# Kernel optimization log

Measured on AMD Instinct MI355X. Metric: run time of the kernel, lower is better.

## Reference

```python
import jax, jax.numpy as jnp
import numpy as np

N = 10000
E = 160000
H = 4
NEG_SLOPE = 0.2


def _edge_softmax(e, dst):
    # e: [E, H] logits; softmax over edges sharing the same dst node
    m = jax.ops.segment_max(e, dst, num_segments=N)          # [N, H]
    m = jnp.where(jnp.isfinite(m), m, 0.0)
    ex = jnp.exp(e - m[dst])                                  # [E, H]
    den = jax.ops.segment_sum(ex, dst, num_segments=N)       # [N, H]
    return ex / (den[dst] + 1e-9)


def _gat_layer(x, src, dst, W, al, ar, resW, edge=None, We=None, ae=None):
    # x: [N, Fin]; W: [Fin, H, D]; al/ar/ae: [H, D]; resW: [Fin, D]
    feat = jnp.einsum('ni,ihd->nhd', x, W)                    # [N, H, D]
    el = jnp.einsum('nhd,hd->nh', feat, al)                   # [N, H]
    er = jnp.einsum('nhd,hd->nh', feat, ar)                   # [N, H]
    e = el[src] + er[dst]                                     # [E, H]
    if edge is not None:
        ef = jnp.einsum('ei,ihd->ehd', edge, We)              # [E, H, D]
        e = e + jnp.einsum('ehd,hd->eh', ef, ae)
    e = jax.nn.leaky_relu(e, NEG_SLOPE)
    alpha = _edge_softmax(e, dst)                             # [E, H]
    msg = feat[src] * alpha[:, :, None]                       # [E, H, D]
    out = jax.ops.segment_sum(msg, dst, num_segments=N)      # [N, H, D]
    return out.mean(axis=1) + x @ resW                        # [N, D]


def setup_inputs() -> dict:
    key = jax.random.key(0)
    ks = jax.random.split(key, 24)
    node_in, edge_in, hid, out = 128, 64, 128, 256
    s = 0.1
    d = {
        'node_feats': jax.random.normal(ks[0], (N, node_in), jnp.float32),
        'edge_feats': jax.random.normal(ks[1], (E, edge_in), jnp.float32),
        'src': jax.random.randint(ks[2], (E,), 0, N, jnp.int32),
        'dst': jax.random.randint(ks[3], (E,), 0, N, jnp.int32),
        # conv1 (with edge feats): node_in -> hid
        'W1':  s * jax.random.normal(ks[4],  (node_in, H, hid), jnp.float32),
        'We1': s * jax.random.normal(ks[5],  (edge_in, H, hid), jnp.float32),
        'al1': s * jax.random.normal(ks[6],  (H, hid), jnp.float32),
        'ar1': s * jax.random.normal(ks[7],  (H, hid), jnp.float32),
        'ae1': s * jax.random.normal(ks[8],  (H, hid), jnp.float32),
        'res1': s * jax.random.normal(ks[9], (node_in, hid), jnp.float32),
        # conv2: hid -> hid
        'W2':  s * jax.random.normal(ks[10], (hid, H, hid), jnp.float32),
        'al2': s * jax.random.normal(ks[11], (H, hid), jnp.float32),
        'ar2': s * jax.random.normal(ks[12], (H, hid), jnp.float32),
        'res2': s * jax.random.normal(ks[13], (hid, hid), jnp.float32),
        # conv3: hid -> hid
        'W3':  s * jax.random.normal(ks[14], (hid, H, hid), jnp.float32),
        'al3': s * jax.random.normal(ks[15], (H, hid), jnp.float32),
        'ar3': s * jax.random.normal(ks[16], (H, hid), jnp.float32),
        'res3': s * jax.random.normal(ks[17], (hid, hid), jnp.float32),
        # conv4: hid -> out
        'W4':  s * jax.random.normal(ks[18], (hid, H, out), jnp.float32),
        'al4': s * jax.random.normal(ks[19], (H, out), jnp.float32),
        'ar4': s * jax.random.normal(ks[20], (H, out), jnp.float32),
        'res4': s * jax.random.normal(ks[21], (hid, out), jnp.float32),
    }
    return d


def reference(node_feats, edge_feats, src, dst,
              W1, We1, al1, ar1, ae1, res1,
              W2, al2, ar2, res2,
              W3, al3, ar3, res3,
              W4, al4, ar4, res4):
    h = jax.nn.relu(_gat_layer(node_feats, src, dst, W1, al1, ar1, res1,
                               edge=edge_feats, We=We1, ae=ae1))
    h = jax.nn.relu(_gat_layer(h, src, dst, W2, al2, ar2, res2))
    h = jax.nn.relu(_gat_layer(h, src, dst, W3, al3, ar3, res3))
    h = jax.nn.relu(_gat_layer(h, src, dst, W4, al4, ar4, res4))
    return h
```

## Files before the change

kernel.cpp:

```cpp
#include <hip/hip_runtime.h>

#define NN 10000
#define EE 160000

typedef __attribute__((ext_vector_type(8))) short bf16x8;
typedef __attribute__((ext_vector_type(4))) float f32x4;

__device__ __forceinline__ float b2f(unsigned short s) {
    union { unsigned u; float f; } v; v.u = ((unsigned)s) << 16; return v.f;
}
__device__ __forceinline__ short f2b(float f) {
    union { float f; unsigned u; } v; v.f = f;
    unsigned r = v.u + 0x7FFF + ((v.u >> 16) & 1);
    return (short)(r >> 16);
}

__global__ __launch_bounds__(256) void hist_kernel(const int* __restrict__ dst,
                                                   int* __restrict__ counts, int E) {
    int e = blockIdx.x * 256 + threadIdx.x;
    if (e < E) atomicAdd(&counts[dst[e]], 1);
}

__global__ __launch_bounds__(256) void scan_kernel(const int* __restrict__ counts,
                                                   int* __restrict__ off,
                                                   int* __restrict__ cur, int n) {
    __shared__ int buf[NN];
    __shared__ int part[256];
    int tid = threadIdx.x;
    for (int j = tid; j < n; j += 256) buf[j] = counts[j];
    __syncthreads();
    int chunk = (n + 255) / 256;
    int lo = tid * chunk; if (lo > n) lo = n;
    int hi = lo + chunk;  if (hi > n) hi = n;
    int s = 0;
    for (int i = lo; i < hi; ++i) s += buf[i];
    part[tid] = s;
    __syncthreads();
    for (int o = 1; o < 256; o <<= 1) {
        int v = (tid >= o) ? part[tid - o] : 0;
        __syncthreads();
        part[tid] += v;
        __syncthreads();
    }
    int run = (tid == 0) ? 0 : part[tid - 1];
    for (int i = lo; i < hi; ++i) { int c = buf[i]; buf[i] = run; run += c; }
    __syncthreads();
    for (int j = tid; j < n; j += 256) { int v = buf[j]; off[j] = v; cur[j] = v; }
    if (tid == 255) off[n] = part[255];
}

__global__ __launch_bounds__(256) void fill_extra(const int* __restrict__ src,
                                                  const int* __restrict__ dst,
                                                  int* __restrict__ cur,
                                                  const float* __restrict__ ef,
                                                  const float* __restrict__ vbuf,
                                                  int* __restrict__ ssrc,
                                                  float* __restrict__ extra, int E) {
    __shared__ float vs[256];
    vs[threadIdx.x] = vbuf[threadIdx.x];
    __syncthreads();
    int e = blockIdx.x * 256 + threadIdx.x;
    if (e >= E) return;
    int p = atomicAdd(&cur[dst[e]], 1);
    ssrc[p] = src[e];
    float a0 = 0.f, a1 = 0.f, a2 = 0.f, a3 = 0.f;
    const float4* e4 = (const float4*)(ef + (size_t)e * 64);
    #pragma unroll
    for (int c = 0; c < 16; ++c) {
        float4 x = e4[c];
        int b = c * 16;
        a0 += x.x * vs[b + 0] + x.y * vs[b + 4] + x.z * vs[b + 8] + x.w * vs[b + 12];
        a1 += x.x * vs[b + 1] + x.y * vs[b + 5] + x.z * vs[b + 9] + x.w * vs[b + 13];
        a2 += x.x * vs[b + 2] + x.y * vs[b + 6] + x.z * vs[b + 10] + x.w * vs[b + 14];
        a3 += x.x * vs[b + 3] + x.y * vs[b + 7] + x.z * vs[b + 11] + x.w * vs[b + 15];
    }
    float4 o; o.x = a0; o.y = a1; o.z = a2; o.w = a3;
    *(float4*)(extra + (size_t)p * 4) = o;
}

struct PrepParams {
    const float* tsrc[8];
    short* tdst[8];
    int tN[8];
    int tshift[8];
    int tcum4[9];
    const float* W[4]; const float* al[4]; const float* ar[4];
    short* Wc[4]; int Dl[4]; int base[4];
    const float* We1; const float* ae1; float* vbuf;
    const float* node_feats; short* xb;
    int* counts;
    int bWA, bV, bC, bZ;
};
__global__ __launch_bounds__(256) void prep_kernel(PrepParams P) {
    int blk = blockIdx.x, tid = threadIdx.x;
    if (blk < P.bWA) {
        int t = blk * 256 + tid;
        if (t >= P.tcum4[8]) return;
        int i = 0;
        #pragma unroll
        for (int j = 1; j < 8; ++j) i += (t >= P.tcum4[j]);
        int local = t - P.tcum4[i];
        int N = P.tN[i], sh = P.tshift[i];
        int k = local >> (sh - 2);
        int nq = local & ((N >> 2) - 1);
        float4 v = *(const float4*)(P.tsrc[i] + (size_t)k * N + nq * 4);
        short* d = P.tdst[i] + (size_t)nq * 4 * 128 + k;
        d[0] = f2b(v.x); d[128] = f2b(v.y); d[256] = f2b(v.z); d[384] = f2b(v.w);
    } else if (blk < P.bV) {
        int bl = blk - P.bWA;
        int l = bl >> 7, within = bl & 127;
        int wv = tid >> 6, ln = tid & 63;
        int wid = within * 4 + wv;
        int k = wid >> 2, h = wid & 3;
        int D = P.Dl[l];
        const float* w = P.W[l] + ((size_t)k * 4 + h) * D;
        const float* a = P.al[l] + (size_t)h * D;
        const float* r = P.ar[l] + (size_t)h * D;
        float sa, sr;
        if (D == 128) {
            float2 w2 = ((const float2*)w)[ln];
            float2 a2 = ((const float2*)a)[ln];
            float2 r2 = ((const float2*)r)[ln];
            sa = w2.x * a2.x + w2.y * a2.y;
            sr = w2.x * r2.x + w2.y * r2.y;
        } else {
            float4 w4 = ((const float4*)w)[ln];
            float4 a4 = ((const float4*)a)[ln];
            float4 r4 = ((const float4*)r)[ln];
            sa = w4.x * a4.x + w4.y * a4.y + w4.z * a4.z + w4.w * a4.w;
            sr = w4.x * r4.x + w4.y * r4.y + w4.z * r4.z + w4.w * r4.w;
        }
        #pragma unroll
        for (int o = 32; o; o >>= 1) { sa += __shfl_xor(sa, o); sr += __shfl_xor(sr, o); }
        if (ln == 0) {
            P.Wc[l][(size_t)(P.base[l] + h) * 128 + k]     = f2b(sa);
            P.Wc[l][(size_t)(P.base[l] + 4 + h) * 128 + k] = f2b(sr);
        }
    } else if (blk < P.bC) {
        int bl = blk - P.bV;
        int wv = tid >> 6, ln = tid & 63;
        int i = bl * 4 + wv;
        #pragma unroll
        for (int h = 0; h < 4; ++h) {
            const float* w = P.We1 + ((size_t)i * 4 + h) * 128;
            const float* a = P.ae1 + (size_t)h * 128;
            float2 w2 = ((const float2*)w)[ln];
            float2 a2 = ((const float2*)a)[ln];
            float s = w2.x * a2.x + w2.y * a2.y;
            #pragma unroll
            for (int o = 32; o; o >>= 1) s += __shfl_xor(s, o);
            if (ln == 0) P.vbuf[i * 4 + h] = s;
        }
    } else if (blk < P.bZ) {
        int t = (blk - P.bC) * 256 + tid;
        if (t < NN * 32) {
            float4 v = ((const float4*)P.node_feats)[t];
            uint2 pk;
            pk.x = (unsigned short)f2b(v.x) | ((unsigned)(unsigned short)f2b(v.y) << 16);
            pk.y = (unsigned short)f2b(v.z) | ((unsigned)(unsigned short)f2b(v.w) << 16);
            ((uint2*)P.xb)[t] = pk;
        }
    } else {
        int t = (blk - P.bZ) * 256 + tid;
        if (t < NN / 4) ((int4*)P.counts)[t] = make_int4(0, 0, 0, 0);
    }
}

template <int D>
__global__ __launch_bounds__(256) void gemm_fused(const short* __restrict__ A,
                                                  const short* __restrict__ Bt,
                                                  short* __restrict__ featb,
                                                  float* __restrict__ y,
                                                  float* __restrict__ elr,
                                                  int M) {
    constexpr int HD = 4 * D;
    int wave = threadIdx.x >> 6, lane = threadIdx.x & 63;
    int m0 = blockIdx.y * 64;
    int n0 = blockIdx.x * 64 + wave * 16;
    int r = lane & 15, quad = lane >> 4;
    f32x4 acc[4] = {};
    const short* bp = Bt + (size_t)(n0 + r) * 128 + quad * 8;
    #pragma unroll
    for (int k0 = 0; k0 < 128; k0 += 32) {
        bf16x8 bfrag = *(const bf16x8*)(bp + k0);
        #pragma unroll
        for (int mt = 0; mt < 4; ++mt) {
            int gm = m0 + mt * 16 + r;
            bf16x8 afrag = {};
            if (gm < M) afrag = *(const bf16x8*)(A + (size_t)gm * 128 + k0 + quad * 8);
            acc[mt] = __builtin_amdgcn_mfma_f32_16x16x32_bf16(afrag, bfrag, acc[mt], 0, 0, 0);
        }
    }
    int col = n0 + r;
    #pragma unroll
    for (int mt = 0; mt < 4; ++mt) {
        #pragma unroll
        for (int rr = 0; rr < 4; ++rr) {
            int gm = m0 + mt * 16 + quad * 4 + rr;
            if (gm >= M) continue;
            float v = acc[mt][rr];
            if (col < HD)              featb[(size_t)gm * HD + col] = f2b(v);
            else if (col < HD + D)     y[(size_t)gm * D + (col - HD)] = v;
            else if (col < HD + D + 8) elr[(size_t)gm * 8 + (col - HD - D)] = v;
        }
    }
}

__device__ __forceinline__ void accum8(float* a, uint4 v, float w) {
    a[0] += w * b2f((unsigned short)(v.x & 0xFFFF));
    a[1] += w * b2f((unsigned short)(v.x >> 16));
    a[2] += w * b2f((unsigned short)(v.y & 0xFFFF));
    a[3] += w * b2f((unsigned short)(v.y >> 16));
    a[4] += w * b2f((unsigned short)(v.z & 0xFFFF));
    a[5] += w * b2f((unsigned short)(v.z >> 16));
    a[6] += w * b2f((unsigned short)(v.w & 0xFFFF));
    a[7] += w * b2f((unsigned short)(v.w >> 16));
}

template <int CH>
__device__ __forceinline__ void gather_chunk(int cnt, int sidx,
                                             float e0, float e1, float e2, float e3,
                                             const short* __restrict__ featb, int ln,
                                             float acc[CH][8]) {
    constexpr int HD = CH * 512;
    const short* base = featb + ln * 8;
    int j = 0;
    for (; j + 2 <= cnt; j += 2) {
        int sA = __shfl(sidx, j), sB = __shfl(sidx, j + 1);
        float wA0 = __shfl(e0, j), wA1 = __shfl(e1, j), wA2 = __shfl(e2, j), wA3 = __shfl(e3, j);
        float wB0 = __shfl(e0, j + 1), wB1 = __shfl(e1, j + 1), wB2 = __shfl(e2, j + 1), wB3 = __shfl(e3, j + 1);
        const short* fA = base + (size_t)sA * HD;
        const short* fB = base + (size_t)sB * HD;
        uint4 vA[CH], vB[CH];
        #pragma unroll
        for (int c = 0; c < CH; ++c) { vA[c] = *(const uint4*)(fA + c * 512); vB[c] = *(const uint4*)(fB + c * 512); }
        #pragma unroll
        for (int c = 0; c < CH; ++c) {
            float wA, wB;
            if (CH == 1) {
                wA = ln < 16 ? wA0 : ln < 32 ? wA1 : ln < 48 ? wA2 : wA3;
                wB = ln < 16 ? wB0 : ln < 32 ? wB1 : ln < 48 ? wB2 : wB3;
            } else {
                wA = (c == 0) ? (ln < 32 ? wA0 : wA1) : (ln < 32 ? wA2 : wA3);
                wB = (c == 0) ? (ln < 32 ? wB0 : wB1) : (ln < 32 ? wB2 : wB3);
            }
            accum8(acc[c], vA[c], wA);
            accum8(acc[c], vB[c], wB);
        }
    }
    if (j < cnt) {
        int sA = __shfl(sidx, j);
        float wA0 = __shfl(e0, j), wA1 = __shfl(e1, j), wA2 = __shfl(e2, j), wA3 = __shfl(e3, j);
        const short* fA = base + (size_t)sA * HD;
        #pragma unroll
        for (int c = 0; c < CH; ++c) {
            uint4 vA = *(const uint4*)(fA + c * 512);
            float wA;
            if (CH == 1) wA = ln < 16 ? wA0 : ln < 32 ? wA1 : ln < 48 ? wA2 : wA3;
            else         wA = (c == 0) ? (ln < 32 ? wA0 : wA1) : (ln < 32 ? wA2 : wA3);
            accum8(acc[c], vA, wA);
        }
    }
}

template <int D, bool HAS_EXTRA, bool WRITE_BF>
__global__ __launch_bounds__(256) void gat_wave(const short* __restrict__ featb,
                                                const float* __restrict__ elr,
                                                const float* __restrict__ extra,
                                                const int* __restrict__ ssrc,
                                                const int* __restrict__ off,
                                                const float* __restrict__ yres,
                                                float* __restrict__ yout,
                                                short* __restrict__ ybf) {
    constexpr int HD = 4 * D;
    constexpr int CH = HD / 512;
    int wv = threadIdx.x >> 6, ln = threadIdx.x & 63;
    int n = blockIdx.x * 4 + wv;
    int r0 = off[n], deg = off[n + 1] - r0;

    float4 erv = *(const float4*)(elr + (size_t)n * 8 + 4);

    float acc[CH][8];
    #pragma unroll
    for (int c = 0; c < CH; ++c)
        #pragma unroll
        for (int i = 0; i < 8; ++i) acc[c][i] = 0.f;

    float sc0, sc1, sc2, sc3;

    auto logits = [&](int idx, float& a0, float& a1, float& a2, float& a3) {
        int s = ssrc[idx];
        float4 elv = *(const float4*)(elr + (size_t)s * 8);
        a0 = elv.x + erv.x; a1 = elv.y + erv.y; a2 = elv.z + erv.z; a3 = elv.w + erv.w;
        if (HAS_EXTRA) {
            float4 exv = *(const float4*)(extra + (size_t)idx * 4);
            a0 += exv.x; a1 += exv.y; a2 += exv.z; a3 += exv.w;
        }
        a0 = a0 > 0.f ? a0 : 0.2f * a0;
        a1 = a1 > 0.f ? a1 : 0.2f * a1;
        a2 = a2 > 0.f ? a2 : 0.2f * a2;
        a3 = a3 > 0.f ? a3 : 0.2f * a3;
        return s;
    };

    if (deg <= 64) {
        int sidx = 0;
        float a0 = -1e30f, a1 = -1e30f, a2 = -1e30f, a3 = -1e30f;
        if (ln < deg) sidx = logits(r0 + ln, a0, a1, a2, a3);
        float m0 = a0, m1 = a1, m2 = a2, m3 = a3;
        #pragma unroll
        for (int o = 32; o; o >>= 1) {
            m0 = fmaxf(m0, __shfl_xor(m0, o)); m1 = fmaxf(m1, __shfl_xor(m1, o));
            m2 = fmaxf(m2, __shfl_xor(m2, o)); m3 = fmaxf(m3, __shfl_xor(m3, o));
        }
        float e0 = 0.f, e1 = 0.f, e2 = 0.f, e3 = 0.f;
        if (ln < deg) {
            e0 = __expf(a0 - m0); e1 = __expf(a1 - m1);
            e2 = __expf(a2 - m2); e3 = __expf(a3 - m3);
        }
        float s0 = e0, s1 = e1, s2 = e2, s3 = e3;
        #pragma unroll
        for (int o = 32; o; o >>= 1) {
            s0 += __shfl_xor(s0, o); s1 += __shfl_xor(s1, o);
            s2 += __shfl_xor(s2, o); s3 += __shfl_xor(s3, o);
        }
        sc0 = 0.25f / (s0 + 1e-9f); sc1 = 0.25f / (s1 + 1e-9f);
        sc2 = 0.25f / (s2 + 1e-9f); sc3 = 0.25f / (s3 + 1e-9f);
        gather_chunk<CH>(deg, sidx, e0, e1, e2, e3, featb, ln, acc);
    } else {
        float m0 = -1e30f, m1 = -1e30f, m2 = -1e30f, m3 = -1e30f;
        for (int base = 0; base < deg; base += 64) {
            float a0 = -1e30f, a1 = -1e30f, a2 = -1e30f, a3 = -1e30f;
            if (base + ln < deg) logits(r0 + base + ln, a0, a1, a2, a3);
            m0 = fmaxf(m0, a0); m1 = fmaxf(m1, a1); m2 = fmaxf(m2, a2); m3 = fmaxf(m3, a3);
        }
        #pragma unroll
        for (int o = 32; o; o >>= 1) {
            m0 = fmaxf(m0, __shfl_xor(m0, o)); m1 = fmaxf(m1, __shfl_xor(m1, o));
            m2 = fmaxf(m2, __shfl_xor(m2, o)); m3 = fmaxf(m3, __shfl_xor(m3, o));
        }
        float s0 = 0.f, s1 = 0.f, s2 = 0.f, s3 = 0.f;
        for (int base = 0; base < deg; base += 64) {
            float a0, a1, a2, a3;
            if (base + ln < deg) {
                logits(r0 + base + ln, a0, a1, a2, a3);
                s0 += __expf(a0 - m0); s1 += __expf(a1 - m1);
                s2 += __expf(a2 - m2); s3 += __expf(a3 - m3);
            }
        }
        #pragma unroll
        for (int o = 32; o; o >>= 1) {
            s0 += __shfl_xor(s0, o); s1 += __shfl_xor(s1, o);
            s2 += __shfl_xor(s2, o); s3 += __shfl_xor(s3, o);
        }
        sc0 = 0.25f / (s0 + 1e-9f); sc1 = 0.25f / (s1 + 1e-9f);
        sc2 = 0.25f / (s2 + 1e-9f); sc3 = 0.25f / (s3 + 1e-9f);
        for (int base = 0; base < deg; base += 64) {
            int sidx = 0;
            float e0 = 0.f, e1 = 0.f, e2 = 0.f, e3 = 0.f;
            if (base + ln < deg) {
                float a0, a1, a2, a3;
                sidx = logits(r0 + base + ln, a0, a1, a2, a3);
                e0 = __expf(a0 - m0); e1 = __expf(a1 - m1);
                e2 = __expf(a2 - m2); e3 = __expf(a3 - m3);
            }
            int cnt = deg - base; if (cnt > 64) cnt = 64;
            gather_chunk<CH>(cnt, sidx, e0, e1, e2, e3, featb, ln, acc);
        }
    }

    if (CH == 1) {
        float scl = ln < 16 ? sc0 : ln < 32 ? sc1 : ln < 48 ? sc2 : sc3;
        float t[8];
        #pragma unroll
        for (int i = 0; i < 8; ++i) {
            float v = acc[0][i] * scl;
            v += __shfl_xor(v, 16);
            v += __shfl_xor(v, 32);
            t[i] = v;
        }
        if (ln < 16) {
            int d0 = ln * 8;
            const float* yr = yres + (size_t)n * D + d0;
            float4 ya = *(const float4*)yr;
            float4 yb = *(const float4*)(yr + 4);
            float o[8];
            o[0] = fmaxf(ya.x + t[0], 0.f); o[1] = fmaxf(ya.y + t[1], 0.f);
            o[2] = fmaxf(ya.z + t[2], 0.f); o[3] = fmaxf(ya.w + t[3], 0.f);
            o[4] = fmaxf(yb.x + t[4], 0.f); o[5] = fmaxf(yb.y + t[5], 0.f);
            o[6] = fmaxf(yb.z + t[6], 0.f); o[7] = fmaxf(yb.w + t[7], 0.f);
            if (WRITE_BF) {
                uint4 pk;
                pk.x = (unsigned short)f2b(o[0]) | ((unsigned)(unsigned short)f2b(o[1]) << 16);
                pk.y = (unsigned short)f2b(o[2]) | ((unsigned)(unsigned short)f2b(o[3]) << 16);
                pk.z = (unsigned short)f2b(o[4]) | ((unsigned)(unsigned short)f2b(o[5]) << 16);
                pk.w = (unsigned short)f2b(o[6]) | ((unsigned)(unsigned short)f2b(o[7]) << 16);
                *(uint4*)(ybf + (size_t)n * D + d0) = pk;
            } else {
                float4 oa, ob;
                oa.x = o[0]; oa.y = o[1]; oa.z = o[2]; oa.w = o[3];
                ob.x = o[4]; ob.y = o[5]; ob.z = o[6]; ob.w = o[7];
                *(float4*)(yout + (size_t)n * D + d0) = oa;
                *(float4*)(yout + (size_t)n * D + d0 + 4) = ob;
            }
        }
    } else {
        float scA = ln < 32 ? sc0 : sc1;
        float scB = ln < 32 ? sc2 : sc3;
        float t[8];
        #pragma unroll
        for (int i = 0; i < 8; ++i) {
            float v = acc[0][i] * scA + acc[1][i] * scB;
            v += __shfl_xor(v, 32);
            t[i] = v;
        }
        if (ln < 32) {
            int d0 = ln * 8;
            const float* yr = yres + (size_t)n * D + d0;
            float4 ya = *(const float4*)yr;
            float4 yb = *(const float4*)(yr + 4);
            float o[8];
            o[0] = fmaxf(ya.x + t[0], 0.f); o[1] = fmaxf(ya.y + t[1], 0.f);
            o[2] = fmaxf(ya.z + t[2], 0.f); o[3] = fmaxf(ya.w + t[3], 0.f);
            o[4] = fmaxf(yb.x + t[4], 0.f); o[5] = fmaxf(yb.y + t[5], 0.f);
            o[6] = fmaxf(yb.z + t[6], 0.f); o[7] = fmaxf(yb.w + t[7], 0.f);
            if (WRITE_BF) {
                uint4 pk;
                pk.x = (unsigned short)f2b(o[0]) | ((unsigned)(unsigned short)f2b(o[1]) << 16);
                pk.y = (unsigned short)f2b(o[2]) | ((unsigned)(unsigned short)f2b(o[3]) << 16);
                pk.z = (unsigned short)f2b(o[4]) | ((unsigned)(unsigned short)f2b(o[5]) << 16);
                pk.w = (unsigned short)f2b(o[6]) | ((unsigned)(unsigned short)f2b(o[7]) << 16);
                *(uint4*)(ybf + (size_t)n * D + d0) = pk;
            } else {
                float4 oa, ob;
                oa.x = o[0]; oa.y = o[1]; oa.z = o[2]; oa.w = o[3];
                ob.x = o[4]; ob.y = o[5]; ob.z = o[6]; ob.w = o[7];
                *(float4*)(yout + (size_t)n * D + d0) = oa;
                *(float4*)(yout + (size_t)n * D + d0 + 4) = ob;
            }
        }
    }
}

extern "C" void kernel_launch(void* const* d_in, const int* in_sizes, int n_in,
                              void* d_out, int out_size, void* d_ws, size_t ws_size,
                              hipStream_t stream) {
    const float* node_feats = (const float*)d_in[0];
    const float* edge_feats = (const float*)d_in[1];
    const int*   src        = (const int*)d_in[2];
    const int*   dst        = (const int*)d_in[3];
    const float* W1   = (const float*)d_in[4];
    const float* We1  = (const float*)d_in[5];
    const float* al1  = (const float*)d_in[6];
    const float* ar1  = (const float*)d_in[7];
    const float* ae1  = (const float*)d_in[8];
    const float* res1 = (const float*)d_in[9];
    const float* W2   = (const float*)d_in[10];
    const float* al2  = (const float*)d_in[11];
    const float* ar2  = (const float*)d_in[12];
    const float* res2 = (const float*)d_in[13];
    const float* W3   = (const float*)d_in[14];
    const float* al3  = (const float*)d_in[15];
    const float* ar3  = (const float*)d_in[16];
    const float* res3 = (const float*)d_in[17];
    const float* W4   = (const float*)d_in[18];
    const float* al4  = (const float*)d_in[19];
    const float* ar4  = (const float*)d_in[20];
    const float* res4 = (const float*)d_in[21];

    char* ws = (char*)d_ws;
    auto alloc = [&](size_t bytes) -> char* {
        char* p = ws;
        ws += (bytes + 255) & ~(size_t)255;
        return p;
    };
    int*   counts  = (int*)alloc((size_t)NN * 4);
    int*   offsets = (int*)alloc((size_t)(NN + 1) * 4);
    int*   cursor  = (int*)alloc((size_t)(NN + 1) * 4);
    int*   ssrc    = (int*)alloc((size_t)EE * 4);
    short* featb   = (short*)alloc((size_t)NN * 1024 * 2);
    float* xA      = (float*)alloc((size_t)NN * 128 * 4);
    short* xb      = (short*)alloc((size_t)NN * 128 * 2);
    float* elr     = (float*)alloc((size_t)NN * 8 * 4);
    float* extra   = (float*)alloc((size_t)EE * 4 * 4);
    float* vbuf    = (float*)alloc(1024);
    short* Wc1     = (short*)alloc((size_t)704 * 128 * 2);
    short* Wc2     = (short*)alloc((size_t)704 * 128 * 2);
    short* Wc3     = (short*)alloc((size_t)704 * 128 * 2);
    short* Wc4     = (short*)alloc((size_t)1344 * 128 * 2);

    PrepParams P;
    P.tsrc[0] = W1;   P.tdst[0] = Wc1;              P.tN[0] = 512;  P.tshift[0] = 9;
    P.tsrc[1] = W2;   P.tdst[1] = Wc2;              P.tN[1] = 512;  P.tshift[1] = 9;
    P.tsrc[2] = W3;   P.tdst[2] = Wc3;              P.tN[2] = 512;  P.tshift[2] = 9;
    P.tsrc[3] = W4;   P.tdst[3] = Wc4;              P.tN[3] = 1024; P.tshift[3] = 10;
    P.tsrc[4] = res1; P.tdst[4] = Wc1 + 512 * 128;  P.tN[4] = 128;  P.tshift[4] = 7;
    P.tsrc[5] = res2; P.tdst[5] = Wc2 + 512 * 128;  P.tN[5] = 128;  P.tshift[5] = 7;
    P.tsrc[6] = res3; P.tdst[6] = Wc3 + 512 * 128;  P.tN[6] = 128;  P.tshift[6] = 7;
    P.tsrc[7] = res4; P.tdst[7] = Wc4 + 1024 * 128; P.tN[7] = 256;  P.tshift[7] = 8;
    P.tcum4[0] = 0;
    for (int i = 0; i < 8; ++i) P.tcum4[i + 1] = P.tcum4[i] + P.tN[i] * 128 / 4;
    P.W[0] = W1; P.W[1] = W2; P.W[2] = W3; P.W[3] = W4;
    P.al[0] = al1; P.al[1] = al2; P.al[2] = al3; P.al[3] = al4;
    P.ar[0] = ar1; P.ar[1] = ar2; P.ar[2] = ar3; P.ar[3] = ar4;
    P.Wc[0] = Wc1; P.Wc[1] = Wc2; P.Wc[2] = Wc3; P.Wc[3] = Wc4;
    P.Dl[0] = 128; P.Dl[1] = 128; P.Dl[2] = 128; P.Dl[3] = 256;
    P.base[0] = 640; P.base[1] = 640; P.base[2] = 640; P.base[3] = 1280;
    P.We1 = We1; P.ae1 = ae1; P.vbuf = vbuf;
    P.node_feats = node_feats; P.xb = xb;
    P.counts = counts;
    P.bWA = (P.tcum4[8] + 255) / 256;
    P.bV  = P.bWA + 512;
    P.bC  = P.bV + 16;
    P.bZ  = P.bC + (NN * 32 + 255) / 256;
    int nblk = P.bZ + (NN / 4 + 255) / 256;
    prep_kernel<<<nblk, 256, 0, stream>>>(P);

    hist_kernel<<<(EE + 255) / 256, 256, 0, stream>>>(dst, counts, EE);
    scan_kernel<<<1, 256, 0, stream>>>(counts, offsets, cursor, NN);
    fill_extra<<<(EE + 255) / 256, 256, 0, stream>>>(src, dst, cursor, edge_feats,
                                                     vbuf, ssrc, extra, EE);

    float* out = (float*)d_out;
    dim3 g128(11, (NN + 63) / 64);
    dim3 g256(21, (NN + 63) / 64);
    int gw = NN / 4;

    gemm_fused<128><<<g128, 256, 0, stream>>>(xb, Wc1, featb, xA, elr, NN);
    gat_wave<128, true, true><<<gw, 256, 0, stream>>>(featb, elr, extra, ssrc, offsets, xA, nullptr, xb);
    gemm_fused<128><<<g128, 256, 0, stream>>>(xb, Wc2, featb, xA, elr, NN);
    gat_wave<128, false, true><<<gw, 256, 0, stream>>>(featb, elr, nullptr, ssrc, offsets, xA, nullptr, xb);
    gemm_fused<128><<<g128, 256, 0, stream>>>(xb, Wc3, featb, xA, elr, NN);
    gat_wave<128, false, true><<<gw, 256, 0, stream>>>(featb, elr, nullptr, ssrc, offsets, xA, nullptr, xb);
    gemm_fused<256><<<g256, 256, 0, stream>>>(xb, Wc4, featb, out, elr, NN);
    gat_wave<256, false, false><<<gw, 256, 0, stream>>>(featb, elr, nullptr, ssrc, offsets, out, out, nullptr);
}
```

Measured before the change: 382.9 us.

## Split each node's GAT aggregation across two waves with LDS reduction

```diff
diff --git a/kernel.cpp b/kernel.cpp
--- a/kernel.cpp
+++ b/kernel.cpp
@@ -217,75 +217,89 @@
     a[7] += w * b2f((unsigned short)(v.w >> 16));
 }
 
-template <int CH>
-__device__ __forceinline__ void gather_chunk(int cnt, int sidx,
-                                             float e0, float e1, float e2, float e3,
-                                             const short* __restrict__ featb, int ln,
-                                             float acc[CH][8]) {
-    constexpr int HD = CH * 512;
-    const short* base = featb + ln * 8;
+__device__ __forceinline__ float sel4(int ln, float s0, float s1, float s2, float s3) {
+    return ln < 16 ? s0 : ln < 32 ? s1 : ln < 48 ? s2 : s3;
+}
+
+__device__ __forceinline__ void gather_q(int cnt, int start, int step, int sidx,
+                                         float e0, float e1, float e2, float e3,
+                                         const short* __restrict__ base, int ln,
+                                         float acc[8]) {
+    int j = start;
+    for (; j + 3 * step < cnt; j += 4 * step) {
+        int jB = j + step, jC = j + 2 * step, jD = j + 3 * step;
+        int s0 = __shfl(sidx, j), s1 = __shfl(sidx, jB);
+        int s2 = __shfl(sidx, jC), s3 = __shfl(sidx, jD);
+        uint4 v0 = *(const uint4*)(base + (size_t)s0 * 512);
+        uint4 v1 = *(const uint4*)(base + (size_t)s1 * 512);
+        uint4 v2 = *(const uint4*)(base + (size_t)s2 * 512);
+        uint4 v3 = *(const uint4*)(base + (size_t)s3 * 512);
+        float a00 = __shfl(e0, j),  a01 = __shfl(e1, j),  a02 = __shfl(e2, j),  a03 = __shfl(e3, j);
+        float a10 = __shfl(e0, jB), a11 = __shfl(e1, jB), a12 = __shfl(e2, jB), a13 = __shfl(e3, jB);
+        float a20 = __shfl(e0, jC), a21 = __shfl(e1, jC), a22 = __shfl(e2, jC), a23 = __shfl(e3, jC);
+        float a30 = __shfl(e0, jD), a31 = __shfl(e1, jD), a32 = __shfl(e2, jD), a33 = __shfl(e3, jD);
+        float w0 = sel4(ln, a00, a01, a02, a03);
+        float w1 = sel4(ln, a10, a11, a12, a13);
+        float w2 = sel4(ln, a20, a21, a22, a23);
+        float w3 = sel4(ln, a30, a31, a32, a33);
+        accum8(acc, v0, w0); accum8(acc, v1, w1);
+        accum8(acc, v2, w2); accum8(acc, v3, w3);
+    }
+    for (; j < cnt; j += step) {
+        int s0 = __shfl(sidx, j);
+        uint4 v0 = *(const uint4*)(base + (size_t)s0 * 512);
+        float a0 = __shfl(e0, j), a1 = __shfl(e1, j), a2 = __shfl(e2, j), a3 = __shfl(e3, j);
+        float w0 = sel4(ln, a0, a1, a2, a3);
+        accum8(acc, v0, w0);
+    }
+}
+
+__device__ __forceinline__ void gather_p(int cnt, int sidx, float eA, float eB,
+                                         const short* __restrict__ base, int ln,
+                                         float acc[8]) {
     int j = 0;
-    for (; j + 2 <= cnt; j += 2) {
-        int sA = __shfl(sidx, j), sB = __shfl(sidx, j + 1);
-        float wA0 = __shfl(e0, j), wA1 = __shfl(e1, j), wA2 = __shfl(e2, j), wA3 = __shfl(e3, j);
-        float wB0 = __shfl(e0, j + 1), wB1 = __shfl(e1, j + 1), wB2 = __shfl(e2, j + 1), wB3 = __shfl(e3, j + 1);
-        const short* fA = base + (size_t)sA * HD;
-        const short* fB = base + (size_t)sB * HD;
-        uint4 vA[CH], vB[CH];
-        #pragma unroll
-        for (int c = 0; c < CH; ++c) { vA[c] = *(const uint4*)(fA + c * 512); vB[c] = *(const uint4*)(fB + c * 512); }
-        #pragma unroll
-        for (int c = 0; c < CH; ++c) {
-            float wA, wB;
-            if (CH == 1) {
-                wA = ln < 16 ? wA0 : ln < 32 ? wA1 : ln < 48 ? wA2 : wA3;
-                wB = ln < 16 ? wB0 : ln < 32 ? wB1 : ln < 48 ? wB2 : wB3;
-            } else {
-                wA = (c == 0) ? (ln < 32 ? wA0 : wA1) : (ln < 32 ? wA2 : wA3);
-                wB = (c == 0) ? (ln < 32 ? wB0 : wB1) : (ln < 32 ? wB2 : wB3);
-            }
-            accum8(acc[c], vA[c], wA);
-            accum8(acc[c], vB[c], wB);
-        }
-    }
-    if (j < cnt) {
-        int sA = __shfl(sidx, j);
-        float wA0 = __shfl(e0, j), wA1 = __shfl(e1, j), wA2 = __shfl(e2, j), wA3 = __shfl(e3, j);
-        const short* fA = base + (size_t)sA * HD;
-        #pragma unroll
-        for (int c = 0; c < CH; ++c) {
-            uint4 vA = *(const uint4*)(fA + c * 512);
-            float wA;
-            if (CH == 1) wA = ln < 16 ? wA0 : ln < 32 ? wA1 : ln < 48 ? wA2 : wA3;
-            else         wA = (c == 0) ? (ln < 32 ? wA0 : wA1) : (ln < 32 ? wA2 : wA3);
-            accum8(acc[c], vA, wA);
-        }
-    }
-}
-
-template <int D, bool HAS_EXTRA, bool WRITE_BF>
-__global__ __launch_bounds__(256) void gat_wave(const short* __restrict__ featb,
-                                                const float* __restrict__ elr,
-                                                const float* __restrict__ extra,
-                                                const int* __restrict__ ssrc,
-                                                const int* __restrict__ off,
-                                                const float* __restrict__ yres,
-                                                float* __restrict__ yout,
-                                                short* __restrict__ ybf) {
-    constexpr int HD = 4 * D;
-    constexpr int CH = HD / 512;
+    for (; j + 4 <= cnt; j += 4) {
+        int s0 = __shfl(sidx, j), s1 = __shfl(sidx, j + 1);
+        int s2 = __shfl(sidx, j + 2), s3 = __shfl(sidx, j + 3);
+        uint4 v0 = *(const uint4*)(base + (size_t)s0 * 1024);
+        uint4 v1 = *(const uint4*)(base + (size_t)s1 * 1024);
+        uint4 v2 = *(const uint4*)(base + (size_t)s2 * 1024);
+        uint4 v3 = *(const uint4*)(base + (size_t)s3 * 1024);
+        float a0A = __shfl(eA, j),     a0B = __shfl(eB, j);
+        float a1A = __shfl(eA, j + 1), a1B = __shfl(eB, j + 1);
+        float a2A = __shfl(eA, j + 2), a2B = __shfl(eB, j + 2);
+        float a3A = __shfl(eA, j + 3), a3B = __shfl(eB, j + 3);
+        float w0 = ln < 32 ? a0A : a0B;
+        float w1 = ln < 32 ? a1A : a1B;
+        float w2 = ln < 32 ? a2A : a2B;
+        float w3 = ln < 32 ? a3A : a3B;
+        accum8(acc, v0, w0); accum8(acc, v1, w1);
+        accum8(acc, v2, w2); accum8(acc, v3, w3);
+    }
+    for (; j < cnt; ++j) {
+        int s0 = __shfl(sidx, j);
+        uint4 v0 = *(const uint4*)(base + (size_t)s0 * 1024);
+        float aA = __shfl(eA, j), aB = __shfl(eB, j);
+        float w0 = ln < 32 ? aA : aB;
+        accum8(acc, v0, w0);
+    }
+}
+
+template <bool HAS_EXTRA>
+__global__ __launch_bounds__(256) void gat128(const short* __restrict__ featb,
+                                              const float* __restrict__ elr,
+                                              const float* __restrict__ extra,
+                                              const int* __restrict__ ssrc,
+                                              const int* __restrict__ off,
+                                              const float* __restrict__ yres,
+                                              short* __restrict__ ybf) {
+    __shared__ float red[2][128];
     int wv = threadIdx.x >> 6, ln = threadIdx.x & 63;
-    int n = blockIdx.x * 4 + wv;
+    int slot = wv >> 1, half = wv & 1;
+    int n = blockIdx.x * 2 + slot;
     int r0 = off[n], deg = off[n + 1] - r0;
-
     float4 erv = *(const float4*)(elr + (size_t)n * 8 + 4);
-
-    float acc[CH][8];
-    #pragma unroll
-    for (int c = 0; c < CH; ++c)
-        #pragma unroll
-        for (int i = 0; i < 8; ++i) acc[c][i] = 0.f;
-
+    float acc[8] = {0.f, 0.f, 0.f, 0.f, 0.f, 0.f, 0.f, 0.f};
     float sc0, sc1, sc2, sc3;
 
     auto logits = [&](int idx, float& a0, float& a1, float& a2, float& a3) {
@@ -326,7 +340,7 @@
         }
         sc0 = 0.25f / (s0 + 1e-9f); sc1 = 0.25f / (s1 + 1e-9f);
         sc2 = 0.25f / (s2 + 1e-9f); sc3 = 0.25f / (s3 + 1e-9f);
-        gather_chunk<CH>(deg, sidx, e0, e1, e2, e3, featb, ln, acc);
+        gather_q(deg, half, 2, sidx, e0, e1, e2, e3, featb + ln * 8, ln, acc);
     } else {
         float m0 = -1e30f, m1 = -1e30f, m2 = -1e30f, m3 = -1e30f;
         for (int base = 0; base < deg; base += 64) {
@@ -365,80 +379,173 @@
                 e2 = __expf(a2 - m2); e3 = __expf(a3 - m3);
             }
             int cnt = deg - base; if (cnt > 64) cnt = 64;
-            gather_chunk<CH>(cnt, sidx, e0, e1, e2, e3, featb, ln, acc);
-        }
-    }
-
-    if (CH == 1) {
-        float scl = ln < 16 ? sc0 : ln < 32 ? sc1 : ln < 48 ? sc2 : sc3;
-        float t[8];
-        #pragma unroll
-        for (int i = 0; i < 8; ++i) {
-            float v = acc[0][i] * scl;
-            v += __shfl_xor(v, 16);
-            v += __shfl_xor(v, 32);
-            t[i] = v;
-        }
-        if (ln < 16) {
-            int d0 = ln * 8;
-            const float* yr = yres + (size_t)n * D + d0;
-            float4 ya = *(const float4*)yr;
-            float4 yb = *(const float4*)(yr + 4);
-            float o[8];
-            o[0] = fmaxf(ya.x + t[0], 0.f); o[1] = fmaxf(ya.y + t[1], 0.f);
-            o[2] = fmaxf(ya.z + t[2], 0.f); o[3] = fmaxf(ya.w + t[3], 0.f);
-            o[4] = fmaxf(yb.x + t[4], 0.f); o[5] = fmaxf(yb.y + t[5], 0.f);
-            o[6] = fmaxf(yb.z + t[6], 0.f); o[7] = fmaxf(yb.w + t[7], 0.f);
-            if (WRITE_BF) {
-                uint4 pk;
-                pk.x = (unsigned short)f2b(o[0]) | ((unsigned)(unsigned short)f2b(o[1]) << 16);
-                pk.y = (unsigned short)f2b(o[2]) | ((unsigned)(unsigned short)f2b(o[3]) << 16);
-                pk.z = (unsigned short)f2b(o[4]) | ((unsigned)(unsigned short)f2b(o[5]) << 16);
-                pk.w = (unsigned short)f2b(o[6]) | ((unsigned)(unsigned short)f2b(o[7]) << 16);
-                *(uint4*)(ybf + (size_t)n * D + d0) = pk;
-            } else {
-                float4 oa, ob;
-                oa.x = o[0]; oa.y = o[1]; oa.z = o[2]; oa.w = o[3];
-                ob.x = o[4]; ob.y = o[5]; ob.z = o[6]; ob.w = o[7];
-                *(float4*)(yout + (size_t)n * D + d0) = oa;
-                *(float4*)(yout + (size_t)n * D + d0 + 4) = ob;
+            gather_q(cnt, half, 2, sidx, e0, e1, e2, e3, featb + ln * 8, ln, acc);
+        }
+    }
+
+    float scl = sel4(ln, sc0, sc1, sc2, sc3);
+    float t[8];
+    #pragma unroll
+    for (int i = 0; i < 8; ++i) {
+        float v = acc[i] * scl;
+        v += __shfl_xor(v, 16);
+        v += __shfl_xor(v, 32);
+        t[i] = v;
+    }
+    if (half == 1 && ln < 16) {
+        #pragma unroll
+        for (int i = 0; i < 8; ++i) red[slot][ln * 8 + i] = t[i];
+    }
+    __syncthreads();
+    if (half == 0 && ln < 16) {
+        int d0 = ln * 8;
+        const float* yr = yres + (size_t)n * 128 + d0;
+        float4 ya = *(const float4*)yr;
+        float4 yb = *(const float4*)(yr + 4);
+        float o[8];
+        o[0] = fmaxf(ya.x + t[0] + red[slot][d0 + 0], 0.f);
+        o[1] = fmaxf(ya.y + t[1] + red[slot][d0 + 1], 0.f);
+        o[2] = fmaxf(ya.z + t[2] + red[slot][d0 + 2], 0.f);
+        o[3] = fmaxf(ya.w + t[3] + red[slot][d0 + 3], 0.f);
+        o[4] = fmaxf(yb.x + t[4] + red[slot][d0 + 4], 0.f);
+        o[5] = fmaxf(yb.y + t[5] + red[slot][d0 + 5], 0.f);
+        o[6] = fmaxf(yb.z + t[6] + red[slot][d0 + 6], 0.f);
+        o[7] = fmaxf(yb.w + t[7] + red[slot][d0 + 7], 0.f);
+        uint4 pk;
+        pk.x = (unsigned short)f2b(o[0]) | ((unsigned)(unsigned short)f2b(o[1]) << 16);
+        pk.y = (unsigned short)f2b(o[2]) | ((unsigned)(unsigned short)f2b(o[3]) << 16);
+        pk.z = (unsigned short)f2b(o[4]) | ((unsigned)(unsigned short)f2b(o[5]) << 16);
+        pk.w = (unsigned short)f2b(o[6]) | ((unsigned)(unsigned short)f2b(o[7]) << 16);
+        *(uint4*)(ybf + (size_t)n * 128 + d0) = pk;
+    }
+}
+
+__global__ __launch_bounds__(256) void gat256(const short* __restrict__ featb,
+                                              const float* __restrict__ elr,
+                                              const int* __restrict__ ssrc,
+                                              const int* __restrict__ off,
+                                              const float* __restrict__ yres,
+                                              float* __restrict__ yout) {
+    __shared__ float red[2][256];
+    int wv = threadIdx.x >> 6, ln = threadIdx.x & 63;
+    int slot = wv >> 1, half = wv & 1;
+    int n = blockIdx.x * 2 + slot;
+    int r0 = off[n], deg = off[n + 1] - r0;
+    float4 erv = *(const float4*)(elr + (size_t)n * 8 + 4);
+    float acc[8] = {0.f, 0.f, 0.f, 0.f, 0.f, 0.f, 0.f, 0.f};
+    float sc0, sc1, sc2, sc3;
+    const short* base = featb + half * 512 + ln * 8;
+
+    auto logits = [&](int idx, float& a0, float& a1, float& a2, float& a3) {
+        int s = ssrc[idx];
+        float4 elv = *(const float4*)(elr + (size_t)s * 8);
+        a0 = elv.x + erv.x; a1 = elv.y + erv.y; a2 = elv.z + erv.z; a3 = elv.w + erv.w;
+        a0 = a0 > 0.f ? a0 : 0.2f * a0;
+        a1 = a1 > 0.f ? a1 : 0.2f * a1;
+        a2 = a2 > 0.f ? a2 : 0.2f * a2;
+        a3 = a3 > 0.f ? a3 : 0.2f * a3;
+        return s;
+    };
+
+    if (deg <= 64) {
+        int sidx = 0;
+        float a0 = -1e30f, a1 = -1e30f, a2 = -1e30f, a3 = -1e30f;
+        if (ln < deg) sidx = logits(r0 + ln, a0, a1, a2, a3);
+        float m0 = a0, m1 = a1, m2 = a2, m3 = a3;
+        #pragma unroll
+        for (int o = 32; o; o >>= 1) {
+            m0 = fmaxf(m0, __shfl_xor(m0, o)); m1 = fmaxf(m1, __shfl_xor(m1, o));
+            m2 = fmaxf(m2, __shfl_xor(m2, o)); m3 = fmaxf(m3, __shfl_xor(m3, o));
+        }
+        float e0 = 0.f, e1 = 0.f, e2 = 0.f, e3 = 0.f;
+        if (ln < deg) {
+            e0 = __expf(a0 - m0); e1 = __expf(a1 - m1);
+            e2 = __expf(a2 - m2); e3 = __expf(a3 - m3);
+        }
+        float s0 = e0, s1 = e1, s2 = e2, s3 = e3;
+        #pragma unroll
+        for (int o = 32; o; o >>= 1) {
+            s0 += __shfl_xor(s0, o); s1 += __shfl_xor(s1, o);
+            s2 += __shfl_xor(s2, o); s3 += __shfl_xor(s3, o);
+        }
+        sc0 = 0.25f / (s0 + 1e-9f); sc1 = 0.25f / (s1 + 1e-9f);
+        sc2 = 0.25f / (s2 + 1e-9f); sc3 = 0.25f / (s3 + 1e-9f);
+        float eA = half ? e2 : e0;
+        float eB = half ? e3 : e1;
+        gather_p(deg, sidx, eA, eB, base, ln, acc);
+    } else {
+        float m0 = -1e30f, m1 = -1e30f, m2 = -1e30f, m3 = -1e30f;
+        for (int b = 0; b < deg; b += 64) {
+            float a0 = -1e30f, a1 = -1e30f, a2 = -1e30f, a3 = -1e30f;
+            if (b + ln < deg) logits(r0 + b + ln, a0, a1, a2, a3);
+            m0 = fmaxf(m0, a0); m1 = fmaxf(m1, a1); m2 = fmaxf(m2, a2); m3 = fmaxf(m3, a3);
+        }
+        #pragma unroll
+        for (int o = 32; o; o >>= 1) {
+            m0 = fmaxf(m0, __shfl_xor(m0, o)); m1 = fmaxf(m1, __shfl_xor(m1, o));
+            m2 = fmaxf(m2, __shfl_xor(m2, o)); m3 = fmaxf(m3, __shfl_xor(m3, o));
+        }
+        float s0 = 0.f, s1 = 0.f, s2 = 0.f, s3 = 0.f;
+        for (int b = 0; b < deg; b += 64) {
+            float a0, a1, a2, a3;
+            if (b + ln < deg) {
+                logits(r0 + b + ln, a0, a1, a2, a3);
+                s0 += __expf(a0 - m0); s1 += __expf(a1 - m1);
+                s2 += __expf(a2 - m2); s3 += __expf(a3 - m3);
             }
         }
-    } else {
-        float scA = ln < 32 ? sc0 : sc1;
-        float scB = ln < 32 ? sc2 : sc3;
-        float t[8];
-        #pragma unroll
-        for (int i = 0; i < 8; ++i) {
-            float v = acc[0][i] * scA + acc[1][i] * scB;
-            v += __shfl_xor(v, 32);
-            t[i] = v;
-        }
-        if (ln < 32) {
-            int d0 = ln * 8;
-            const float* yr = yres + (size_t)n * D + d0;
-            float4 ya = *(const float4*)yr;
-            float4 yb = *(const float4*)(yr + 4);
-            float o[8];
-            o[0] = fmaxf(ya.x + t[0], 0.f); o[1] = fmaxf(ya.y + t[1], 0.f);
-            o[2] = fmaxf(ya.z + t[2], 0.f); o[3] = fmaxf(ya.w + t[3], 0.f);
-            o[4] = fmaxf(yb.x + t[4], 0.f); o[5] = fmaxf(yb.y + t[5], 0.f);
-            o[6] = fmaxf(yb.z + t[6], 0.f); o[7] = fmaxf(yb.w + t[7], 0.f);
-            if (WRITE_BF) {
-                uint4 pk;
-                pk.x = (unsigned short)f2b(o[0]) | ((unsigned)(unsigned short)f2b(o[1]) << 16);
-                pk.y = (unsigned short)f2b(o[2]) | ((unsigned)(unsigned short)f2b(o[3]) << 16);
-                pk.z = (unsigned short)f2b(o[4]) | ((unsigned)(unsigned short)f2b(o[5]) << 16);
-                pk.w = (unsigned short)f2b(o[6]) | ((unsigned)(unsigned short)f2b(o[7]) << 16);
-                *(uint4*)(ybf + (size_t)n * D + d0) = pk;
-            } else {
-                float4 oa, ob;
-                oa.x = o[0]; oa.y = o[1]; oa.z = o[2]; oa.w = o[3];
-                ob.x = o[4]; ob.y = o[5]; ob.z = o[6]; ob.w = o[7];
-                *(float4*)(yout + (size_t)n * D + d0) = oa;
-                *(float4*)(yout + (size_t)n * D + d0 + 4) = ob;
+        #pragma unroll
+        for (int o = 32; o; o >>= 1) {
+            s0 += __shfl_xor(s0, o); s1 += __shfl_xor(s1, o);
+            s2 += __shfl_xor(s2, o); s3 += __shfl_xor(s3, o);
+        }
+        sc0 = 0.25f / (s0 + 1e-9f); sc1 = 0.25f / (s1 + 1e-9f);
+        sc2 = 0.25f / (s2 + 1e-9f); sc3 = 0.25f / (s3 + 1e-9f);
+        for (int b = 0; b < deg; b += 64) {
+            int sidx = 0;
+            float e0 = 0.f, e1 = 0.f, e2 = 0.f, e3 = 0.f;
+            if (b + ln < deg) {
+                float a0, a1, a2, a3;
+                sidx = logits(r0 + b + ln, a0, a1, a2, a3);
+                e0 = __expf(a0 - m0); e1 = __expf(a1 - m1);
+                e2 = __expf(a2 - m2); e3 = __expf(a3 - m3);
             }
-        }
+            int cnt = deg - b; if (cnt > 64) cnt = 64;
+            float eA = half ? e2 : e0;
+            float eB = half ? e3 : e1;
+            gather_p(cnt, sidx, eA, eB, base, ln, acc);
+        }
+    }
+
+    float sc = (ln < 32) ? (half ? sc2 : sc0) : (half ? sc3 : sc1);
+    float t[8];
+    #pragma unroll
+    for (int i = 0; i < 8; ++i) {
+        float v = acc[i] * sc;
+        v += __shfl_xor(v, 32);
+        t[i] = v;
+    }
+    if (half == 1 && ln < 32) {
+        #pragma unroll
+        for (int i = 0; i < 8; ++i) red[slot][ln * 8 + i] = t[i];
+    }
+    __syncthreads();
+    if (half == 0 && ln < 32) {
+        int d0 = ln * 8;
+        const float* yr = yres + (size_t)n * 256 + d0;
+        float4 ya = *(const float4*)yr;
+        float4 yb = *(const float4*)(yr + 4);
+        float4 oa, ob;
+        oa.x = fmaxf(ya.x + t[0] + red[slot][d0 + 0], 0.f);
+        oa.y = fmaxf(ya.y + t[1] + red[slot][d0 + 1], 0.f);
+        oa.z = fmaxf(ya.z + t[2] + red[slot][d0 + 2], 0.f);
+        oa.w = fmaxf(ya.w + t[3] + red[slot][d0 + 3], 0.f);
+        ob.x = fmaxf(yb.x + t[4] + red[slot][d0 + 4], 0.f);
+        ob.y = fmaxf(yb.y + t[5] + red[slot][d0 + 5], 0.f);
+        ob.z = fmaxf(yb.z + t[6] + red[slot][d0 + 6], 0.f);
+        ob.w = fmaxf(yb.w + t[7] + red[slot][d0 + 7], 0.f);
+        *(float4*)(yout + (size_t)n * 256 + d0) = oa;
+        *(float4*)(yout + (size_t)n * 256 + d0 + 4) = ob;
     }
 }
 
@@ -524,14 +631,14 @@
     float* out = (float*)d_out;
     dim3 g128(11, (NN + 63) / 64);
     dim3 g256(21, (NN + 63) / 64);
-    int gw = NN / 4;
+    int gs = NN / 2;
 
     gemm_fused<128><<<g128, 256, 0, stream>>>(xb, Wc1, featb, xA, elr, NN);
-    gat_wave<128, true, true><<<gw, 256, 0, stream>>>(featb, elr, extra, ssrc, offsets, xA, nullptr, xb);
+    gat128<true><<<gs, 256, 0, stream>>>(featb, elr, extra, ssrc, offsets, xA, xb);
     gemm_fused<128><<<g128, 256, 0, stream>>>(xb, Wc2, featb, xA, elr, NN);
-    gat_wave<128, false, true><<<gw, 256, 0, stream>>>(featb, elr, nullptr, ssrc, offsets, xA, nullptr, xb);
+    gat128<false><<<gs, 256, 0, stream>>>(featb, elr, nullptr, ssrc, offsets, xA, xb);
     gemm_fused<128><<<g128, 256, 0, stream>>>(xb, Wc3, featb, xA, elr, NN);
-    gat_wave<128, false, true><<<gw, 256, 0, stream>>>(featb, elr, nullptr, ssrc, offsets, xA, nullptr, xb);
+    gat128<false><<<gs, 256, 0, stream>>>(featb, elr, nullptr, ssrc, offsets, xA, xb);
     gemm_fused<256><<<g256, 256, 0, stream>>>(xb, Wc4, featb, out, elr, NN);
-    gat_wave<256, false, false><<<gw, 256, 0, stream>>>(featb, elr, nullptr, ssrc, offsets, out, out, nullptr);
-}
+    gat256<<<gs, 256, 0, stream>>>(featb, elr, ssrc, offsets, out, out);
+}
```

Result: slower. 401.2 us (+4.8%).
